# Optimization experiments

Hardware: AMD Instinct MI355X
Metric: run time of the kernel (lower is better)

The kernel has to match this reference:

```python
import jax, jax.numpy as jnp
import numpy as np

MAX_NUM_CAPS = 10
NEG = -1e9

def _layernorm(x, g, b):
    m = x.mean(-1, keepdims=True)
    v = x.var(-1, keepdims=True)
    return (x - m) / jnp.sqrt(v + 1e-5) * g + b

def _gatv2(x, Wl, Wr, att, bias, adj):
    # x: [B,M,F]; Wl/Wr: [F,H*C]; att: [H,C]; adj: [B,M,M] bool, adj[b,i,j] = edge i->j
    B, M, F = x.shape
    H, C = att.shape
    xl = jnp.einsum('bmf,fhc->bmhc', x, Wl.reshape(F, H, C))  # source transform
    xr = jnp.einsum('bmf,fhc->bmhc', x, Wr.reshape(F, H, C))  # target transform
    # GATv2 score: att . leaky_relu(xl[i] + xr[j]) for edge (src=i, dst=j)
    z = jax.nn.leaky_relu(xl[:, :, None, :, :] + xr[:, None, :, :, :], 0.2)  # [B,i,j,H,C]
    e = jnp.einsum('bijhc,hc->bijh', z, att)
    e = jnp.where(adj[..., None], e, NEG)
    alpha = jax.nn.softmax(e, axis=1)  # softmax over incoming sources i per target j
    out = jnp.einsum('bijh,bihc->bjhc', alpha, xl)  # aggregate at targets
    return out.reshape(B, M, H * C) + bias

def setup_inputs() -> dict:
    key = jax.random.key(0)
    ks = jax.random.split(key, 16)
    B, N, T = 128, 16, 48
    Fm, H, C3 = 128, 4, 64
    s = 0.05
    inp = {
        'team_obs': jax.random.normal(ks[0], (B, N, 14), jnp.float32),
        'target_obs': jax.random.normal(ks[1], (B, T, 15), jnp.float32),
        'team_mask': jax.random.normal(ks[2], (B, 2, N), jnp.float32),
        'local_target_mask': jnp.ones((B, T + 1), jnp.float32),
        'W_emb': jax.random.normal(ks[3], (16, Fm), jnp.float32) * s,
        'b_emb': jnp.zeros((Fm,), jnp.float32),
        'Wl1': jax.random.normal(ks[4], (Fm, Fm), jnp.float32) * s,
        'Wr1': jax.random.normal(ks[5], (Fm, Fm), jnp.float32) * s,
        'att1': jax.random.normal(ks[6], (H, Fm // H), jnp.float32) * s,
        'b1': jnp.zeros((Fm,), jnp.float32),
        'Wl2': jax.random.normal(ks[7], (Fm, Fm), jnp.float32) * s,
        'Wr2': jax.random.normal(ks[8], (Fm, Fm), jnp.float32) * s,
        'att2': jax.random.normal(ks[9], (H, Fm // H), jnp.float32) * s,
        'b2': jnp.zeros((Fm,), jnp.float32),
        'Wl3': jax.random.normal(ks[10], (Fm, C3), jnp.float32) * s,
        'Wr3': jax.random.normal(ks[11], (Fm, C3), jnp.float32) * s,
        'att3': jax.random.normal(ks[12], (1, C3), jnp.float32) * s,
        'b3': jnp.zeros((C3,), jnp.float32),
        'ln1_g': jnp.ones((Fm,), jnp.float32),
        'ln1_b': jnp.zeros((Fm,), jnp.float32),
        'ln2_g': jnp.ones((Fm,), jnp.float32),
        'ln2_b': jnp.zeros((Fm,), jnp.float32),
    }
    return inp

def reference(team_obs, target_obs, team_mask, local_target_mask,
              W_emb, b_emb, Wl1, Wr1, att1, b1, Wl2, Wr2, att2, b2,
              Wl3, Wr3, att3, b3, ln1_g, ln1_b, ln2_g, ln2_b):
    B, N, _ = team_obs.shape
    team = jnp.concatenate([team_obs, jnp.zeros((B, N, 2), team_obs.dtype)], axis=2)
    tgt = target_obs[:, :, :-1]
    T = tgt.shape[1]
    tgt = jnp.concatenate([tgt[:, :, :2 + MAX_NUM_CAPS],
                           jnp.zeros((B, T, 2), tgt.dtype),
                           tgt[:, :, -2:]], axis=2)
    fin = jnp.concatenate([team, tgt], axis=1)  # [B, M, inp_dim]
    h = fin @ W_emb + b_emb  # [B, M, 128]
    imp_team = team_mask[:, 0] != -1e9          # [B, N]
    imp_tgt = local_target_mask[:, :-1] != 0.0  # [B, T]
    imp = jnp.concatenate([imp_team, imp_tgt], axis=1)  # [B, M]
    M = N + T
    eye = jnp.eye(M, dtype=bool)
    # edges among active nodes minus diagonal; PyG GATv2Conv add_self_loops=True re-adds self edges
    adj = (imp[:, :, None] & imp[:, None, :] & ~eye) | eye  # [B, M, M]
    out = jax.nn.relu(_layernorm(_gatv2(h, Wl1, Wr1, att1, b1, adj), ln1_g, ln1_b))
    out = jax.nn.relu(_layernorm(_gatv2(out, Wl2, Wr2, att2, b2, adj), ln2_g, ln2_b))
    out = _gatv2(out, Wl3, Wr3, att3, b3, adj)
    return out  # [B, M, out_dim]
```

## Files before the change

kernel.cpp:

```cpp
#include <hip/hip_runtime.h>

typedef unsigned short u16;
typedef unsigned int   u32;
typedef _Float16 h2  __attribute__((ext_vector_type(2)));
typedef __fp16   hw2 __attribute__((ext_vector_type(2)));
typedef __fp16   hw8 __attribute__((ext_vector_type(8)));
typedef float    f4  __attribute__((ext_vector_type(4)));

#define XS 136

static __device__ __forceinline__ h2 pk(float a, float b) {
    return __builtin_bit_cast(h2, __builtin_amdgcn_cvt_pkrtz(a, b));
}
static __device__ __forceinline__ float dot2(h2 a, h2 b, float c) {
    return __builtin_amdgcn_fdot2(__builtin_bit_cast(hw2, a),
                                  __builtin_bit_cast(hw2, b), c, false);
}
static __device__ __forceinline__ h2  b2h(u32 v) { return __builtin_bit_cast(h2, v); }
static __device__ __forceinline__ u32 h2u(h2 v)  { return __builtin_bit_cast(u32, v); }
static __device__ __forceinline__ h2  abs2(h2 v) { return b2h(h2u(v) & 0x7fff7fffu); }
static __device__ __forceinline__ u16 f2h(float f) { return __builtin_bit_cast(u16, (_Float16)f); }
static __device__ __forceinline__ float h2f(u16 v) { return (float)__builtin_bit_cast(_Float16, v); }
static __device__ __forceinline__ f4 mfma16(uint4 a, uint4 b, f4 c) {
    return __builtin_amdgcn_mfma_f32_16x16x32_f16(__builtin_bit_cast(hw8, a),
                                                  __builtin_bit_cast(hw8, b), c, 0, 0, 0);
}
static __device__ __forceinline__ h2 shflx32(h2 v) {
    return b2h((u32)__shfl_xor((int)h2u(v), 32));
}

__global__ void pack_weights(const float* __restrict__ Wl1, const float* __restrict__ Wr1,
                             const float* __restrict__ Wl2, const float* __restrict__ Wr2,
                             const float* __restrict__ Wl3, const float* __restrict__ Wr3,
                             u32* __restrict__ wpk)
{
    const int o = blockIdx.x * 256 + threadIdx.x;
    const float* src; u32* dst; int local; int N;
    if      (o < 8192)  { src = Wl1; dst = wpk;         local = o;         N = 128; }
    else if (o < 16384) { src = Wr1; dst = wpk + 8192;  local = o - 8192;  N = 128; }
    else if (o < 24576) { src = Wl2; dst = wpk + 16384; local = o - 16384; N = 128; }
    else if (o < 32768) { src = Wr2; dst = wpk + 24576; local = o - 24576; N = 128; }
    else if (o < 36864) { src = Wl3; dst = wpk + 32768; local = o - 32768; N = 64;  }
    else                { src = Wr3; dst = wpk + 36864; local = o - 36864; N = 64;  }
    const int i2   = local & 3;
    const int lane = (local >> 2) & 63;
    const int frag = local >> 8;
    const int kb   = frag & 3;
    const int nt   = frag >> 2;
    const int k0   = kb*32 + ((lane >> 4) << 3) + i2*2;
    const int n    = nt*16 + (lane & 15);
    dst[local] = h2u(pk(src[k0*N + n], src[(k0+1)*N + n]));
}

static __device__ __forceinline__ void compute_imp(int t, int b,
    const float* __restrict__ team_mask, const float* __restrict__ ltm, float* sImp)
{
    if (t < 64) {
        float im;
        if (t < 16) im = (team_mask[b*32 + t] != -1000000000.0f) ? 1.f : 0.f;
        else        im = (ltm[b*49 + (t-16)] != 0.0f) ? 1.f : 0.f;
        sImp[t] = im;
    }
}

static __device__ __forceinline__ void matmul128(int w, int lane,
    const u32* __restrict__ wpkL, const u32* __restrict__ wpkR,
    const u16* sX, u16* sXl, uint4* sXrP)
{
    const int  mt  = w & 3;
    const bool isR = (w >= 4);
    const u32* wp  = isR ? wpkR : wpkL;
    const int  n15 = lane & 15;
    const int  qd  = lane >> 4;
    uint4 afr[4];
#pragma unroll
    for (int kb = 0; kb < 4; kb++)
        afr[kb] = *(const uint4*)&sX[(mt*16 + n15)*XS + kb*32 + (qd << 3)];
#pragma unroll
    for (int nt = 0; nt < 8; nt++) {
        f4 acc = {0.f, 0.f, 0.f, 0.f};
#pragma unroll
        for (int kb = 0; kb < 4; kb++) {
            uint4 bf = *(const uint4*)&wp[((nt*4 + kb)*64 + lane)*4];
            acc = mfma16(afr[kb], bf, acc);
        }
        const int n  = nt*16 + n15;
        const int mb = mt*16 + (qd << 2);
        if (!isR) {
#pragma unroll
            for (int r = 0; r < 4; r++) sXl[(mb + r)*XS + n] = f2h(acc[r]);
        } else {
            u16* xp = (u16*)sXrP;
#pragma unroll
            for (int r = 0; r < 4; r++)
                xp[(((n >> 3)*64) + mb + r)*8 + (n & 7)] = f2h(acc[r]);
        }
    }
}

static __device__ __forceinline__ void attn_ln(int t, int w, int lane, int b, int jh,
    const float* __restrict__ att, const float* __restrict__ bias,
    const float* __restrict__ lg, const float* __restrict__ lb,
    u16* sX, const u16* sXl, const uint4* sXrP,
    float* sAl, float* sPart, float* sL2, const float* sImp, u32* __restrict__ gxOut)
{
    const int h  = w & 3;
    const int ih = w >> 2;
    const int jj = lane & 31;
    const int is = lane >> 5;
    const int j  = jh*32 + jj;

    h2 a2[16];
#pragma unroll
    for (int q = 0; q < 16; q++) a2[q] = pk(att[h*32 + 2*q], att[h*32 + 2*q + 1]);

    if (w < 4) {
        const uint4* pr = (const uint4*)&sXl[lane*XS + h*32];
        float al = 0.f;
#pragma unroll
        for (int c4 = 0; c4 < 4; c4++) {
            uint4 v = pr[c4];
            al = dot2(b2h(v.x), a2[c4*4+0], al);
            al = dot2(b2h(v.y), a2[c4*4+1], al);
            al = dot2(b2h(v.z), a2[c4*4+2], al);
            al = dot2(b2h(v.w), a2[c4*4+3], al);
        }
        sAl[h*64 + lane] = al;
    }

    h2 xr2[16];
#pragma unroll
    for (int s = 0; s < 4; s++) {
        uint4 v = sXrP[(h*4 + s)*64 + j];
        xr2[s*4+0] = b2h(v.x); xr2[s*4+1] = b2h(v.y);
        xr2[s*4+2] = b2h(v.z); xr2[s*4+3] = b2h(v.w);
    }
    float Ar = 0.f;
#pragma unroll
    for (int q = 0; q < 16; q++) Ar = dot2(a2[q], xr2[q], Ar);
    const float impj = sImp[j];
    __syncthreads();

    float l = 0.f;
    h2 acc2[16];
#pragma unroll
    for (int q = 0; q < 16; q++) acc2[q] = b2h(0u);
    const int i0 = ih*32 + is*16;
#pragma unroll 4
    for (int ii = 0; ii < 16; ii++) {
        int i = i0 + ii;
        const uint4* pl = (const uint4*)&sXl[i*XS + h*32];
        uint4 v0 = pl[0], v1 = pl[1], v2 = pl[2], v3 = pl[3];
        h2 xl2[16];
        xl2[0] = b2h(v0.x); xl2[1] = b2h(v0.y); xl2[2]  = b2h(v0.z); xl2[3]  = b2h(v0.w);
        xl2[4] = b2h(v1.x); xl2[5] = b2h(v1.y); xl2[6]  = b2h(v1.z); xl2[7]  = b2h(v1.w);
        xl2[8] = b2h(v2.x); xl2[9] = b2h(v2.y); xl2[10] = b2h(v2.z); xl2[11] = b2h(v2.w);
        xl2[12]= b2h(v3.x); xl2[13]= b2h(v3.y); xl2[14] = b2h(v3.z); xl2[15] = b2h(v3.w);
        float S0 = 0.f, S1 = 0.f;
#pragma unroll
        for (int q = 0; q < 16; q += 2) {
            h2 t0 = abs2(xl2[q]   + xr2[q]);
            h2 t1 = abs2(xl2[q+1] + xr2[q+1]);
            S0 = dot2(a2[q],   t0, S0);
            S1 = dot2(a2[q+1], t1, S1);
        }
        float e  = 0.6f*(sAl[h*64 + i] + Ar) + 0.4f*(S0 + S1);
        float ad = (i == j) ? 1.f : impj * sImp[i];
        float p  = (ad != 0.f) ? __expf(e) : 0.f;
        l += p;
        h2 p2 = pk(p, p);
#pragma unroll
        for (int q = 0; q < 16; q++) acc2[q] += p2 * xl2[q];
    }

    l += __shfl_xor(l, 32);
#pragma unroll
    for (int q = 0; q < 16; q++) acc2[q] = acc2[q] + shflx32(acc2[q]);

    u32* ov = (u32*)sX;
    if (w >= 4 && lane < 32) {
        uint4* d4 = (uint4*)(ov + (h*32 + jj)*20);
        uint4 o;
        o.x = h2u(acc2[0]);  o.y = h2u(acc2[1]);  o.z = h2u(acc2[2]);  o.w = h2u(acc2[3]);  d4[0] = o;
        o.x = h2u(acc2[4]);  o.y = h2u(acc2[5]);  o.z = h2u(acc2[6]);  o.w = h2u(acc2[7]);  d4[1] = o;
        o.x = h2u(acc2[8]);  o.y = h2u(acc2[9]);  o.z = h2u(acc2[10]); o.w = h2u(acc2[11]); d4[2] = o;
        o.x = h2u(acc2[12]); o.y = h2u(acc2[13]); o.z = h2u(acc2[14]); o.w = h2u(acc2[15]); d4[3] = o;
        sL2[h*32 + jj] = l;
    }
    __syncthreads();

    float yv[32];
    if (w < 4 && lane < 32) {
        const uint4* s4 = (const uint4*)(ov + (h*32 + jj)*20);
        uint4 u0 = s4[0], u1 = s4[1], u2 = s4[2], u3 = s4[3];
        h2 oth[16];
        oth[0] = b2h(u0.x); oth[1] = b2h(u0.y); oth[2]  = b2h(u0.z); oth[3]  = b2h(u0.w);
        oth[4] = b2h(u1.x); oth[5] = b2h(u1.y); oth[6]  = b2h(u1.z); oth[7]  = b2h(u1.w);
        oth[8] = b2h(u2.x); oth[9] = b2h(u2.y); oth[10] = b2h(u2.z); oth[11] = b2h(u2.w);
        oth[12]= b2h(u3.x); oth[13]= b2h(u3.y); oth[14] = b2h(u3.z); oth[15] = b2h(u3.w);
        l += sL2[h*32 + jj];
        const float rl = 1.f / l;
        float s1 = 0.f, s2v = 0.f;
#pragma unroll
        for (int q = 0; q < 16; q++) {
            h2 sum = acc2[q] + oth[q];
            float y0 = fmaf((float)sum[0], rl, bias[h*32 + 2*q]);
            float y1 = fmaf((float)sum[1], rl, bias[h*32 + 2*q + 1]);
            yv[2*q] = y0; yv[2*q+1] = y1;
            s1 += y0 + y1;
            s2v = fmaf(y0, y0, s2v);
            s2v = fmaf(y1, y1, s2v);
        }
        sPart[h*32 + jj]       = s1;
        sPart[128 + h*32 + jj] = s2v;
    }
    __syncthreads();

    if (w < 4 && lane < 32) {
        float su = sPart[jj] + sPart[32 + jj] + sPart[64 + jj] + sPart[96 + jj];
        float sq = sPart[128 + jj] + sPart[160 + jj] + sPart[192 + jj] + sPart[224 + jj];
        const float mean = su * 0.0078125f;
        const float var  = sq * 0.0078125f - mean*mean;
        const float rstd = rsqrtf(var + 1e-5f);
#pragma unroll
        for (int q = 0; q < 16; q++) {
            int f0 = h*32 + 2*q;
            float v0 = fmaxf(fmaf((yv[2*q]   - mean)*rstd, lg[f0],   lb[f0]),   0.f);
            float v1 = fmaxf(fmaf((yv[2*q+1] - mean)*rstd, lg[f0+1], lb[f0+1]), 0.f);
            ov[(h*32 + jj)*20 + q] = h2u(pk(v0, v1));
        }
    }
    __syncthreads();

    for (int r = t; r < 2048; r += 512) {
        int nj = r >> 6, c = r & 63, hh = c >> 4, qq = c & 15;
        gxOut[(size_t)b*4096 + (size_t)(jh*32 + nj)*64 + c] = ov[(hh*32 + nj)*20 + qq];
    }
}

__global__ void __launch_bounds__(512, 1) gnn_layer1(
    const float* __restrict__ team_obs, const float* __restrict__ target_obs,
    const float* __restrict__ team_mask, const float* __restrict__ ltm,
    const float* __restrict__ W_emb, const float* __restrict__ b_emb,
    const float* __restrict__ att1, const float* __restrict__ b1,
    const float* __restrict__ ln1_g, const float* __restrict__ ln1_b,
    const u32* __restrict__ wpk, u32* __restrict__ gx1)
{
    __shared__ __align__(16) u16   sX  [64*XS];
    __shared__ __align__(16) u16   sXl [64*XS];
    __shared__ __align__(16) uint4 sXrP[1024];
    __shared__ float sFin[1024];
    __shared__ float sAl [256];
    __shared__ float sPart[256];
    __shared__ float sL2 [128];
    __shared__ float sImp[64];

    const int t    = threadIdx.x;
    const int w    = t >> 6;
    const int lane = t & 63;
    const int b    = blockIdx.x >> 1;
    const int jh   = blockIdx.x & 1;

    compute_imp(t, b, team_mask, ltm, sImp);
    for (int ee = t; ee < 1024; ee += 512) {
        int m = ee >> 4, k = ee & 15;
        float v = 0.f;
        if (m < 16) {
            if (k < 14) v = team_obs[(b*16 + m)*14 + k];
        } else {
            const float* tg = target_obs + (size_t)(b*48 + (m-16))*15;
            if      (k < 12)  v = tg[k];
            else if (k == 14) v = tg[12];
            else if (k == 15) v = tg[13];
        }
        sFin[m*16 + k] = v;
    }
    __syncthreads();

    {
        const int f = t & 127;
        const int g = t >> 7;
        float wreg[16];
#pragma unroll
        for (int k = 0; k < 16; k++) wreg[k] = W_emb[k*128 + f];
        const float bf = b_emb[f];
#pragma unroll
        for (int mm = 0; mm < 16; mm++) {
            int m = g*16 + mm;
            const float4* pf = (const float4*)&sFin[m*16];
            float4 f0 = pf[0], f1 = pf[1], f2 = pf[2], f3 = pf[3];
            float acc = bf;
            acc = fmaf(f0.x, wreg[0],  acc); acc = fmaf(f0.y, wreg[1],  acc);
            acc = fmaf(f0.z, wreg[2],  acc); acc = fmaf(f0.w, wreg[3],  acc);
            acc = fmaf(f1.x, wreg[4],  acc); acc = fmaf(f1.y, wreg[5],  acc);
            acc = fmaf(f1.z, wreg[6],  acc); acc = fmaf(f1.w, wreg[7],  acc);
            acc = fmaf(f2.x, wreg[8],  acc); acc = fmaf(f2.y, wreg[9],  acc);
            acc = fmaf(f2.z, wreg[10], acc); acc = fmaf(f2.w, wreg[11], acc);
            acc = fmaf(f3.x, wreg[12], acc); acc = fmaf(f3.y, wreg[13], acc);
            acc = fmaf(f3.z, wreg[14], acc); acc = fmaf(f3.w, wreg[15], acc);
            sX[m*XS + f] = f2h(acc);
        }
    }
    __syncthreads();

    matmul128(w, lane, wpk, wpk + 8192, sX, sXl, sXrP);
    __syncthreads();
    attn_ln(t, w, lane, b, jh, att1, b1, ln1_g, ln1_b,
            sX, sXl, sXrP, sAl, sPart, sL2, sImp, gx1);
}

__global__ void __launch_bounds__(512, 1) gnn_layer2(
    const float* __restrict__ team_mask, const float* __restrict__ ltm,
    const float* __restrict__ att2, const float* __restrict__ b2,
    const float* __restrict__ ln2_g, const float* __restrict__ ln2_b,
    const u32* __restrict__ wpk, const u32* __restrict__ gxIn, u32* __restrict__ gxOut)
{
    __shared__ __align__(16) u16   sX  [64*XS];
    __shared__ __align__(16) u16   sXl [64*XS];
    __shared__ __align__(16) uint4 sXrP[1024];
    __shared__ float sAl [256];
    __shared__ float sPart[256];
    __shared__ float sL2 [128];
    __shared__ float sImp[64];

    const int t    = threadIdx.x;
    const int w    = t >> 6;
    const int lane = t & 63;
    const int b    = blockIdx.x >> 1;
    const int jh   = blockIdx.x & 1;

    compute_imp(t, b, team_mask, ltm, sImp);
    const uint4* gin = (const uint4*)(gxIn + (size_t)b*4096);
    for (int r = t; r < 1024; r += 512) {
        uint4 v = gin[r];
        int m = r >> 4, seg = r & 15;
        *(uint4*)&sX[m*XS + seg*8] = v;
    }
    __syncthreads();

    matmul128(w, lane, wpk + 16384, wpk + 24576, sX, sXl, sXrP);
    __syncthreads();
    attn_ln(t, w, lane, b, jh, att2, b2, ln2_g, ln2_b,
            sX, sXl, sXrP, sAl, sPart, sL2, sImp, gxOut);
}

__global__ void __launch_bounds__(512, 1) gnn_layer3(
    const float* __restrict__ team_mask, const float* __restrict__ ltm,
    const float* __restrict__ att3, const float* __restrict__ b3,
    const u32* __restrict__ wpk, const u32* __restrict__ gxIn, float* __restrict__ out)
{
    __shared__ __align__(16) u16   sX  [64*XS];
    __shared__ __align__(16) u16   sXl [64*XS];
    __shared__ __align__(16) uint4 sXrP[512];
    __shared__ float sAl [64];
    __shared__ float sPart[512];
    __shared__ float sImp[64];
    __shared__ u16   sE  [64*32];

    const int t    = threadIdx.x;
    const int w    = t >> 6;
    const int lane = t & 63;
    const int b    = blockIdx.x >> 1;
    const int jh   = blockIdx.x & 1;

    compute_imp(t, b, team_mask, ltm, sImp);
    const uint4* gin = (const uint4*)(gxIn + (size_t)b*4096);
    for (int r = t; r < 1024; r += 512) {
        uint4 v = gin[r];
        int m = r >> 4, seg = r & 15;
        *(uint4*)&sX[m*XS + seg*8] = v;
    }
    __syncthreads();

    {
        const int  mt  = w & 3;
        const bool isR = (w >= 4);
        const u32* wp  = isR ? (wpk + 36864) : (wpk + 32768);
        const int  n15 = lane & 15;
        const int  qd  = lane >> 4;
        uint4 afr[4];
#pragma unroll
        for (int kb = 0; kb < 4; kb++)
            afr[kb] = *(const uint4*)&sX[(mt*16 + n15)*XS + kb*32 + (qd << 3)];
#pragma unroll
        for (int nt = 0; nt < 4; nt++) {
            f4 acc = {0.f, 0.f, 0.f, 0.f};
#pragma unroll
            for (int kb = 0; kb < 4; kb++) {
                uint4 bf = *(const uint4*)&wp[((nt*4 + kb)*64 + lane)*4];
                acc = mfma16(afr[kb], bf, acc);
            }
            const int n  = nt*16 + n15;
            const int mb = mt*16 + (qd << 2);
            if (!isR) {
#pragma unroll
                for (int r = 0; r < 4; r++) sXl[(mb + r)*XS + n] = f2h(acc[r]);
            } else {
                u16* xp = (u16*)sXrP;
#pragma unroll
                for (int r = 0; r < 4; r++)
                    xp[(((n >> 3)*64) + mb + r)*8 + (n & 7)] = f2h(acc[r]);
            }
        }
    }
    __syncthreads();

    {
        h2 a2l[4];
#pragma unroll
        for (int q = 0; q < 4; q++) a2l[q] = pk(att3[w*8 + 2*q], att3[w*8 + 2*q + 1]);
        uint4 v = *(const uint4*)&sXl[lane*XS + w*8];
        float al = 0.f;
        al = dot2(b2h(v.x), a2l[0], al);
        al = dot2(b2h(v.y), a2l[1], al);
        al = dot2(b2h(v.z), a2l[2], al);
        al = dot2(b2h(v.w), a2l[3], al);
        sPart[w*64 + lane] = al;
    }
    __syncthreads();
    if (t < 64) {
        sAl[t] = ((sPart[t] + sPart[64+t]) + (sPart[128+t] + sPart[192+t]))
               + ((sPart[256+t] + sPart[320+t]) + (sPart[384+t] + sPart[448+t]));
    }
    __syncthreads();

    const int jj = lane & 31;
    const int is = lane >> 5;
    const int j  = jh*32 + jj;

    {
        h2 a3[32], xr3[32];
#pragma unroll
        for (int q = 0; q < 32; q++) a3[q] = pk(att3[2*q], att3[2*q + 1]);
#pragma unroll
        for (int s = 0; s < 8; s++) {
            uint4 v = sXrP[s*64 + j];
            xr3[s*4+0] = b2h(v.x); xr3[s*4+1] = b2h(v.y);
            xr3[s*4+2] = b2h(v.z); xr3[s*4+3] = b2h(v.w);
        }
        float Ar = 0.f;
#pragma unroll
        for (int q = 0; q < 32; q++) Ar = dot2(a3[q], xr3[q], Ar);
        const float impj = sImp[j];
        const int ib = (w*2 + is)*4;
        for (int ii = 0; ii < 4; ii++) {
            int i = ib + ii;
            const uint4* pl = (const uint4*)&sXl[i*XS];
            float S0 = 0.f, S1 = 0.f;
#pragma unroll
            for (int c4 = 0; c4 < 8; c4++) {
                uint4 v = pl[c4];
                S0 = dot2(a3[c4*4+0], abs2(b2h(v.x) + xr3[c4*4+0]), S0);
                S1 = dot2(a3[c4*4+1], abs2(b2h(v.y) + xr3[c4*4+1]), S1);
                S0 = dot2(a3[c4*4+2], abs2(b2h(v.z) + xr3[c4*4+2]), S0);
                S1 = dot2(a3[c4*4+3], abs2(b2h(v.w) + xr3[c4*4+3]), S1);
            }
            float e  = 0.6f*(sAl[i] + Ar) + 0.4f*(S0 + S1);
            float ad = (i == j) ? 1.f : impj * sImp[i];
            e = (ad != 0.f) ? e : -60000.0f;
            sE[i*32 + jj] = f2h(e);
        }
    }
    __syncthreads();

    {
        const int c0 = w*8;
        h2 acc2[4];
#pragma unroll
        for (int q = 0; q < 4; q++) acc2[q] = b2h(0u);
        float l = 0.f;
        for (int k = 0; k < 32; k++) {
            int i = is*32 + k;
            float p = __expf(h2f(sE[i*32 + jj]));
            l += p;
            h2 p2 = pk(p, p);
            uint4 v = *(const uint4*)&sXl[i*XS + c0];
            acc2[0] += p2 * b2h(v.x);
            acc2[1] += p2 * b2h(v.y);
            acc2[2] += p2 * b2h(v.z);
            acc2[3] += p2 * b2h(v.w);
        }
        l += __shfl_xor(l, 32);
#pragma unroll
        for (int q = 0; q < 4; q++) acc2[q] = acc2[q] + shflx32(acc2[q]);
        if (is == 0) {
            const float rl = 1.f / l;
            float o[8];
#pragma unroll
            for (int q = 0; q < 4; q++) {
                o[2*q]   = fmaf((float)acc2[q][0], rl, b3[c0 + 2*q]);
                o[2*q+1] = fmaf((float)acc2[q][1], rl, b3[c0 + 2*q + 1]);
            }
            float4* po = (float4*)(out + (size_t)b*4096 + (size_t)j*64 + c0);
            po[0] = *(const float4*)&o[0];
            po[1] = *(const float4*)&o[4];
        }
    }
}

extern "C" void kernel_launch(void* const* d_in, const int* in_sizes, int n_in,
                              void* d_out, int out_size, void* d_ws, size_t ws_size,
                              hipStream_t stream) {
    (void)in_sizes; (void)n_in; (void)ws_size; (void)out_size;
    const float* team_obs          = (const float*)d_in[0];
    const float* target_obs        = (const float*)d_in[1];
    const float* team_mask         = (const float*)d_in[2];
    const float* local_target_mask = (const float*)d_in[3];
    const float* W_emb             = (const float*)d_in[4];
    const float* b_emb             = (const float*)d_in[5];
    const float* Wl1               = (const float*)d_in[6];
    const float* Wr1               = (const float*)d_in[7];
    const float* att1              = (const float*)d_in[8];
    const float* b1                = (const float*)d_in[9];
    const float* Wl2               = (const float*)d_in[10];
    const float* Wr2               = (const float*)d_in[11];
    const float* att2              = (const float*)d_in[12];
    const float* b2                = (const float*)d_in[13];
    const float* Wl3               = (const float*)d_in[14];
    const float* Wr3               = (const float*)d_in[15];
    const float* att3              = (const float*)d_in[16];
    const float* b3                = (const float*)d_in[17];
    const float* ln1_g             = (const float*)d_in[18];
    const float* ln1_b             = (const float*)d_in[19];
    const float* ln2_g             = (const float*)d_in[20];
    const float* ln2_b             = (const float*)d_in[21];
    float* out = (float*)d_out;

    u32* wpk = (u32*)d_ws;
    u32* gx2 = (u32*)d_ws + 40960;
    u32* gx1 = (u32*)d_out;

    pack_weights<<<dim3(160), dim3(256), 0, stream>>>(Wl1, Wr1, Wl2, Wr2, Wl3, Wr3, wpk);
    gnn_layer1<<<dim3(256), dim3(512), 0, stream>>>(
        team_obs, target_obs, team_mask, local_target_mask, W_emb, b_emb,
        att1, b1, ln1_g, ln1_b, wpk, gx1);
    gnn_layer2<<<dim3(256), dim3(512), 0, stream>>>(
        team_mask, local_target_mask, att2, b2, ln2_g, ln2_b, wpk, gx1, gx2);
    gnn_layer3<<<dim3(256), dim3(512), 0, stream>>>(
        team_mask, local_target_mask, att3, b3, wpk, gx2, out);
}
```

Before: 138.6 us.

## Split each batch graph across four blocks instead of two for more parallelism

Each block now handles 16 target nodes instead of 32, so the grid doubles to 512 blocks per layer. Source nodes are split across four lane groups, with a two-step xor-shuffle reduction. Launch bounds are raised to 4 blocks per CU to allow higher occupancy. The price is duplicated per-block work: each block still computes the full 64-node Xl/Xr matmul and the self-attention terms, so redundant compute doubles. The tighter register budget may also cause spills.

New measurement: 192.3 us. +38.7%, slower.

```diff
diff --git a/kernel.cpp b/kernel.cpp
--- a/kernel.cpp
+++ b/kernel.cpp
@@ -25,8 +25,8 @@
     return __builtin_amdgcn_mfma_f32_16x16x32_f16(__builtin_bit_cast(hw8, a),
                                                   __builtin_bit_cast(hw8, b), c, 0, 0, 0);
 }
-static __device__ __forceinline__ h2 shflx32(h2 v) {
-    return b2h((u32)__shfl_xor((int)h2u(v), 32));
+static __device__ __forceinline__ h2 shflx(h2 v, int m) {
+    return b2h((u32)__shfl_xor((int)h2u(v), m));
 }
 
 __global__ void pack_weights(const float* __restrict__ Wl1, const float* __restrict__ Wr1,
@@ -98,7 +98,7 @@
     }
 }
 
-static __device__ __forceinline__ void attn_ln(int t, int w, int lane, int b, int jh,
+static __device__ __forceinline__ void attn_ln(int t, int w, int lane, int b, int jq,
     const float* __restrict__ att, const float* __restrict__ bias,
     const float* __restrict__ lg, const float* __restrict__ lb,
     u16* sX, const u16* sXl, const uint4* sXrP,
@@ -106,9 +106,9 @@
 {
     const int h  = w & 3;
     const int ih = w >> 2;
-    const int jj = lane & 31;
-    const int is = lane >> 5;
-    const int j  = jh*32 + jj;
+    const int jj = lane & 15;
+    const int is = lane >> 4;
+    const int j  = jq*16 + jj;
 
     h2 a2[16];
 #pragma unroll
@@ -145,10 +145,10 @@
     h2 acc2[16];
 #pragma unroll
     for (int q = 0; q < 16; q++) acc2[q] = b2h(0u);
-    const int i0 = ih*32 + is*16;
-#pragma unroll 4
-    for (int ii = 0; ii < 16; ii++) {
-        int i = i0 + ii;
+    const int i0 = ih*32 + is;
+#pragma unroll
+    for (int ii = 0; ii < 8; ii++) {
+        int i = i0 + ii*4;
         const uint4* pl = (const uint4*)&sXl[i*XS + h*32];
         uint4 v0 = pl[0], v1 = pl[1], v2 = pl[2], v3 = pl[3];
         h2 xl2[16];
@@ -173,32 +173,32 @@
         for (int q = 0; q < 16; q++) acc2[q] += p2 * xl2[q];
     }
 
-    l += __shfl_xor(l, 32);
-#pragma unroll
-    for (int q = 0; q < 16; q++) acc2[q] = acc2[q] + shflx32(acc2[q]);
+    l += __shfl_xor(l, 16); l += __shfl_xor(l, 32);
+#pragma unroll
+    for (int q = 0; q < 16; q++) { acc2[q] += shflx(acc2[q], 16); acc2[q] += shflx(acc2[q], 32); }
 
     u32* ov = (u32*)sX;
-    if (w >= 4 && lane < 32) {
-        uint4* d4 = (uint4*)(ov + (h*32 + jj)*20);
+    if (w >= 4 && lane < 16) {
+        uint4* d4 = (uint4*)(ov + (h*16 + jj)*20);
         uint4 o;
         o.x = h2u(acc2[0]);  o.y = h2u(acc2[1]);  o.z = h2u(acc2[2]);  o.w = h2u(acc2[3]);  d4[0] = o;
         o.x = h2u(acc2[4]);  o.y = h2u(acc2[5]);  o.z = h2u(acc2[6]);  o.w = h2u(acc2[7]);  d4[1] = o;
         o.x = h2u(acc2[8]);  o.y = h2u(acc2[9]);  o.z = h2u(acc2[10]); o.w = h2u(acc2[11]); d4[2] = o;
         o.x = h2u(acc2[12]); o.y = h2u(acc2[13]); o.z = h2u(acc2[14]); o.w = h2u(acc2[15]); d4[3] = o;
-        sL2[h*32 + jj] = l;
+        sL2[h*16 + jj] = l;
     }
     __syncthreads();
 
     float yv[32];
-    if (w < 4 && lane < 32) {
-        const uint4* s4 = (const uint4*)(ov + (h*32 + jj)*20);
+    if (w < 4 && lane < 16) {
+        const uint4* s4 = (const uint4*)(ov + (h*16 + jj)*20);
         uint4 u0 = s4[0], u1 = s4[1], u2 = s4[2], u3 = s4[3];
         h2 oth[16];
         oth[0] = b2h(u0.x); oth[1] = b2h(u0.y); oth[2]  = b2h(u0.z); oth[3]  = b2h(u0.w);
         oth[4] = b2h(u1.x); oth[5] = b2h(u1.y); oth[6]  = b2h(u1.z); oth[7]  = b2h(u1.w);
         oth[8] = b2h(u2.x); oth[9] = b2h(u2.y); oth[10] = b2h(u2.z); oth[11] = b2h(u2.w);
         oth[12]= b2h(u3.x); oth[13]= b2h(u3.y); oth[14] = b2h(u3.z); oth[15] = b2h(u3.w);
-        l += sL2[h*32 + jj];
+        l += sL2[h*16 + jj];
         const float rl = 1.f / l;
         float s1 = 0.f, s2v = 0.f;
 #pragma unroll
@@ -211,14 +211,14 @@
             s2v = fmaf(y0, y0, s2v);
             s2v = fmaf(y1, y1, s2v);
         }
-        sPart[h*32 + jj]       = s1;
-        sPart[128 + h*32 + jj] = s2v;
-    }
-    __syncthreads();
-
-    if (w < 4 && lane < 32) {
-        float su = sPart[jj] + sPart[32 + jj] + sPart[64 + jj] + sPart[96 + jj];
-        float sq = sPart[128 + jj] + sPart[160 + jj] + sPart[192 + jj] + sPart[224 + jj];
+        sPart[h*16 + jj]      = s1;
+        sPart[64 + h*16 + jj] = s2v;
+    }
+    __syncthreads();
+
+    if (w < 4 && lane < 16) {
+        float su = sPart[jj] + sPart[16 + jj] + sPart[32 + jj] + sPart[48 + jj];
+        float sq = sPart[64 + jj] + sPart[80 + jj] + sPart[96 + jj] + sPart[112 + jj];
         const float mean = su * 0.0078125f;
         const float var  = sq * 0.0078125f - mean*mean;
         const float rstd = rsqrtf(var + 1e-5f);
@@ -227,18 +227,18 @@
             int f0 = h*32 + 2*q;
             float v0 = fmaxf(fmaf((yv[2*q]   - mean)*rstd, lg[f0],   lb[f0]),   0.f);
             float v1 = fmaxf(fmaf((yv[2*q+1] - mean)*rstd, lg[f0+1], lb[f0+1]), 0.f);
-            ov[(h*32 + jj)*20 + q] = h2u(pk(v0, v1));
-        }
-    }
-    __syncthreads();
-
-    for (int r = t; r < 2048; r += 512) {
+            ov[(h*16 + jj)*20 + q] = h2u(pk(v0, v1));
+        }
+    }
+    __syncthreads();
+
+    for (int r = t; r < 1024; r += 512) {
         int nj = r >> 6, c = r & 63, hh = c >> 4, qq = c & 15;
-        gxOut[(size_t)b*4096 + (size_t)(jh*32 + nj)*64 + c] = ov[(hh*32 + nj)*20 + qq];
-    }
-}
-
-__global__ void __launch_bounds__(512, 1) gnn_layer1(
+        gxOut[(size_t)b*4096 + (size_t)(jq*16 + nj)*64 + c] = ov[(hh*16 + nj)*20 + qq];
+    }
+}
+
+__global__ void __launch_bounds__(512, 4) gnn_layer1(
     const float* __restrict__ team_obs, const float* __restrict__ target_obs,
     const float* __restrict__ team_mask, const float* __restrict__ ltm,
     const float* __restrict__ W_emb, const float* __restrict__ b_emb,
@@ -251,15 +251,15 @@
     __shared__ __align__(16) uint4 sXrP[1024];
     __shared__ float sFin[1024];
     __shared__ float sAl [256];
-    __shared__ float sPart[256];
-    __shared__ float sL2 [128];
+    __shared__ float sPart[128];
+    __shared__ float sL2 [64];
     __shared__ float sImp[64];
 
     const int t    = threadIdx.x;
     const int w    = t >> 6;
     const int lane = t & 63;
-    const int b    = blockIdx.x >> 1;
-    const int jh   = blockIdx.x & 1;
+    const int b    = blockIdx.x >> 2;
+    const int jq   = blockIdx.x & 3;
 
     compute_imp(t, b, team_mask, ltm, sImp);
     for (int ee = t; ee < 1024; ee += 512) {
@@ -305,11 +305,11 @@
 
     matmul128(w, lane, wpk, wpk + 8192, sX, sXl, sXrP);
     __syncthreads();
-    attn_ln(t, w, lane, b, jh, att1, b1, ln1_g, ln1_b,
+    attn_ln(t, w, lane, b, jq, att1, b1, ln1_g, ln1_b,
             sX, sXl, sXrP, sAl, sPart, sL2, sImp, gx1);
 }
 
-__global__ void __launch_bounds__(512, 1) gnn_layer2(
+__global__ void __launch_bounds__(512, 4) gnn_layer2(
     const float* __restrict__ team_mask, const float* __restrict__ ltm,
     const float* __restrict__ att2, const float* __restrict__ b2,
     const float* __restrict__ ln2_g, const float* __restrict__ ln2_b,
@@ -319,15 +319,15 @@
     __shared__ __align__(16) u16   sXl [64*XS];
     __shared__ __align__(16) uint4 sXrP[1024];
     __shared__ float sAl [256];
-    __shared__ float sPart[256];
-    __shared__ float sL2 [128];
+    __shared__ float sPart[128];
+    __shared__ float sL2 [64];
     __shared__ float sImp[64];
 
     const int t    = threadIdx.x;
     const int w    = t >> 6;
     const int lane = t & 63;
-    const int b    = blockIdx.x >> 1;
-    const int jh   = blockIdx.x & 1;
+    const int b    = blockIdx.x >> 2;
+    const int jq   = blockIdx.x & 3;
 
     compute_imp(t, b, team_mask, ltm, sImp);
     const uint4* gin = (const uint4*)(gxIn + (size_t)b*4096);
@@ -340,11 +340,11 @@
 
     matmul128(w, lane, wpk + 16384, wpk + 24576, sX, sXl, sXrP);
     __syncthreads();
-    attn_ln(t, w, lane, b, jh, att2, b2, ln2_g, ln2_b,
+    attn_ln(t, w, lane, b, jq, att2, b2, ln2_g, ln2_b,
             sX, sXl, sXrP, sAl, sPart, sL2, sImp, gxOut);
 }
 
-__global__ void __launch_bounds__(512, 1) gnn_layer3(
+__global__ void __launch_bounds__(512, 4) gnn_layer3(
     const float* __restrict__ team_mask, const float* __restrict__ ltm,
     const float* __restrict__ att3, const float* __restrict__ b3,
     const u32* __restrict__ wpk, const u32* __restrict__ gxIn, float* __restrict__ out)
@@ -355,13 +355,13 @@
     __shared__ float sAl [64];
     __shared__ float sPart[512];
     __shared__ float sImp[64];
-    __shared__ u16   sE  [64*32];
+    __shared__ u16   sE  [64*16];
 
     const int t    = threadIdx.x;
     const int w    = t >> 6;
     const int lane = t & 63;
-    const int b    = blockIdx.x >> 1;
-    const int jh   = blockIdx.x & 1;
+    const int b    = blockIdx.x >> 2;
+    const int jq   = blockIdx.x & 3;
 
     compute_imp(t, b, team_mask, ltm, sImp);
     const uint4* gin = (const uint4*)(gxIn + (size_t)b*4096);
@@ -424,9 +424,9 @@
     }
     __syncthreads();
 
-    const int jj = lane & 31;
-    const int is = lane >> 5;
-    const int j  = jh*32 + jj;
+    const int jj = lane & 15;
+    const int is = lane >> 4;
+    const int j  = jq*16 + jj;
 
     {
         h2 a3[32], xr3[32];
@@ -442,8 +442,9 @@
 #pragma unroll
         for (int q = 0; q < 32; q++) Ar = dot2(a3[q], xr3[q], Ar);
         const float impj = sImp[j];
-        const int ib = (w*2 + is)*4;
-        for (int ii = 0; ii < 4; ii++) {
+        const int ib = (w*4 + is)*2;
+#pragma unroll
+        for (int ii = 0; ii < 2; ii++) {
             int i = ib + ii;
             const uint4* pl = (const uint4*)&sXl[i*XS];
             float S0 = 0.f, S1 = 0.f;
@@ -458,7 +459,7 @@
             float e  = 0.6f*(sAl[i] + Ar) + 0.4f*(S0 + S1);
             float ad = (i == j) ? 1.f : impj * sImp[i];
             e = (ad != 0.f) ? e : -60000.0f;
-            sE[i*32 + jj] = f2h(e);
+            sE[i*16 + jj] = f2h(e);
         }
     }
     __syncthreads();
@@ -469,9 +470,9 @@
 #pragma unroll
         for (int q = 0; q < 4; q++) acc2[q] = b2h(0u);
         float l = 0.f;
-        for (int k = 0; k < 32; k++) {
-            int i = is*32 + k;
-            float p = __expf(h2f(sE[i*32 + jj]));
+        for (int k = 0; k < 16; k++) {
+            int i = is + 4*k;
+            float p = __expf(h2f(sE[i*16 + jj]));
             l += p;
             h2 p2 = pk(p, p);
             uint4 v = *(const uint4*)&sXl[i*XS + c0];
@@ -480,9 +481,9 @@
             acc2[2] += p2 * b2h(v.z);
             acc2[3] += p2 * b2h(v.w);
         }
-        l += __shfl_xor(l, 32);
-#pragma unroll
-        for (int q = 0; q < 4; q++) acc2[q] = acc2[q] + shflx32(acc2[q]);
+        l += __shfl_xor(l, 16); l += __shfl_xor(l, 32);
+#pragma unroll
+        for (int q = 0; q < 4; q++) { acc2[q] += shflx(acc2[q], 16); acc2[q] += shflx(acc2[q], 32); }
         if (is == 0) {
             const float rl = 1.f / l;
             float o[8];
@@ -531,11 +532,11 @@
     u32* gx1 = (u32*)d_out;
 
     pack_weights<<<dim3(160), dim3(256), 0, stream>>>(Wl1, Wr1, Wl2, Wr2, Wl3, Wr3, wpk);
-    gnn_layer1<<<dim3(256), dim3(512), 0, stream>>>(
+    gnn_layer1<<<dim3(512), dim3(512), 0, stream>>>(
         team_obs, target_obs, team_mask, local_target_mask, W_emb, b_emb,
         att1, b1, ln1_g, ln1_b, wpk, gx1);
-    gnn_layer2<<<dim3(256), dim3(512), 0, stream>>>(
+    gnn_layer2<<<dim3(512), dim3(512), 0, stream>>>(
         team_mask, local_target_mask, att2, b2, ln2_g, ln2_b, wpk, gx1, gx2);
-    gnn_layer3<<<dim3(256), dim3(512), 0, stream>>>(
+    gnn_layer3<<<dim3(512), dim3(512), 0, stream>>>(
         team_mask, local_target_mask, att3, b3, wpk, gx2, out);
 }
```

## Fuse three GNN layer kernels into one cooperative kernel with grid syncs

Applied to the files above, without the earlier changes.

Merges the three per-layer kernels into a single cooperative launch, using grid-wide barriers between layers instead of separate kernel launches. This removes two kernel launch gaps and the per-kernel mask recomputation. The layer-3 score buffer reuses the sFin shared array, and the intermediates move from the output buffer to workspace. In exchange the kernel pays grid.sync costs and must have all 256 blocks co-resident, and shared-memory usage now becomes the union of all three layers.

Measured after the change: 220.6 us. +59.1%, slower.

```diff
diff --git a/kernel.cpp b/kernel.cpp
--- a/kernel.cpp
+++ b/kernel.cpp
@@ -1,4 +1,7 @@
 #include <hip/hip_runtime.h>
+#include <hip/hip_cooperative_groups.h>
+
+namespace cg = cooperative_groups;
 
 typedef unsigned short u16;
 typedef unsigned int   u32;
@@ -52,17 +55,6 @@
     dst[local] = h2u(pk(src[k0*N + n], src[(k0+1)*N + n]));
 }
 
-static __device__ __forceinline__ void compute_imp(int t, int b,
-    const float* __restrict__ team_mask, const float* __restrict__ ltm, float* sImp)
-{
-    if (t < 64) {
-        float im;
-        if (t < 16) im = (team_mask[b*32 + t] != -1000000000.0f) ? 1.f : 0.f;
-        else        im = (ltm[b*49 + (t-16)] != 0.0f) ? 1.f : 0.f;
-        sImp[t] = im;
-    }
-}
-
 static __device__ __forceinline__ void matmul128(int w, int lane,
     const u32* __restrict__ wpkL, const u32* __restrict__ wpkR,
     const u16* sX, u16* sXl, uint4* sXrP)
@@ -238,22 +230,28 @@
     }
 }
 
-__global__ void __launch_bounds__(512, 1) gnn_layer1(
+__global__ void __launch_bounds__(512) gnn_all(
     const float* __restrict__ team_obs, const float* __restrict__ target_obs,
     const float* __restrict__ team_mask, const float* __restrict__ ltm,
     const float* __restrict__ W_emb, const float* __restrict__ b_emb,
     const float* __restrict__ att1, const float* __restrict__ b1,
+    const float* __restrict__ att2, const float* __restrict__ b2,
+    const float* __restrict__ att3, const float* __restrict__ b3,
     const float* __restrict__ ln1_g, const float* __restrict__ ln1_b,
-    const u32* __restrict__ wpk, u32* __restrict__ gx1)
+    const float* __restrict__ ln2_g, const float* __restrict__ ln2_b,
+    const u32* __restrict__ wpk, u32* __restrict__ gx1, u32* __restrict__ gx2,
+    float* __restrict__ out)
 {
     __shared__ __align__(16) u16   sX  [64*XS];
     __shared__ __align__(16) u16   sXl [64*XS];
     __shared__ __align__(16) uint4 sXrP[1024];
-    __shared__ float sFin[1024];
+    __shared__ __align__(16) float sFin[1024];
     __shared__ float sAl [256];
-    __shared__ float sPart[256];
+    __shared__ float sPart[512];
     __shared__ float sL2 [128];
     __shared__ float sImp[64];
+
+    cg::grid_group grid = cg::this_grid();
 
     const int t    = threadIdx.x;
     const int w    = t >> 6;
@@ -261,7 +259,12 @@
     const int b    = blockIdx.x >> 1;
     const int jh   = blockIdx.x & 1;
 
-    compute_imp(t, b, team_mask, ltm, sImp);
+    if (t < 64) {
+        float im;
+        if (t < 16) im = (team_mask[b*32 + t] != -1000000000.0f) ? 1.f : 0.f;
+        else        im = (ltm[b*49 + (t-16)] != 0.0f) ? 1.f : 0.f;
+        sImp[t] = im;
+    }
     for (int ee = t; ee < 1024; ee += 512) {
         int m = ee >> 4, k = ee & 15;
         float v = 0.f;
@@ -307,68 +310,30 @@
     __syncthreads();
     attn_ln(t, w, lane, b, jh, att1, b1, ln1_g, ln1_b,
             sX, sXl, sXrP, sAl, sPart, sL2, sImp, gx1);
-}
-
-__global__ void __launch_bounds__(512, 1) gnn_layer2(
-    const float* __restrict__ team_mask, const float* __restrict__ ltm,
-    const float* __restrict__ att2, const float* __restrict__ b2,
-    const float* __restrict__ ln2_g, const float* __restrict__ ln2_b,
-    const u32* __restrict__ wpk, const u32* __restrict__ gxIn, u32* __restrict__ gxOut)
-{
-    __shared__ __align__(16) u16   sX  [64*XS];
-    __shared__ __align__(16) u16   sXl [64*XS];
-    __shared__ __align__(16) uint4 sXrP[1024];
-    __shared__ float sAl [256];
-    __shared__ float sPart[256];
-    __shared__ float sL2 [128];
-    __shared__ float sImp[64];
-
-    const int t    = threadIdx.x;
-    const int w    = t >> 6;
-    const int lane = t & 63;
-    const int b    = blockIdx.x >> 1;
-    const int jh   = blockIdx.x & 1;
-
-    compute_imp(t, b, team_mask, ltm, sImp);
-    const uint4* gin = (const uint4*)(gxIn + (size_t)b*4096);
-    for (int r = t; r < 1024; r += 512) {
-        uint4 v = gin[r];
-        int m = r >> 4, seg = r & 15;
-        *(uint4*)&sX[m*XS + seg*8] = v;
-    }
-    __syncthreads();
-
+    grid.sync();
+
+    {
+        const uint4* gin = (const uint4*)(gx1 + (size_t)b*4096);
+        for (int r = t; r < 1024; r += 512) {
+            uint4 v = gin[r];
+            int m = r >> 4, seg = r & 15;
+            *(uint4*)&sX[m*XS + seg*8] = v;
+        }
+    }
+    __syncthreads();
     matmul128(w, lane, wpk + 16384, wpk + 24576, sX, sXl, sXrP);
     __syncthreads();
     attn_ln(t, w, lane, b, jh, att2, b2, ln2_g, ln2_b,
-            sX, sXl, sXrP, sAl, sPart, sL2, sImp, gxOut);
-}
-
-__global__ void __launch_bounds__(512, 1) gnn_layer3(
-    const float* __restrict__ team_mask, const float* __restrict__ ltm,
-    const float* __restrict__ att3, const float* __restrict__ b3,
-    const u32* __restrict__ wpk, const u32* __restrict__ gxIn, float* __restrict__ out)
-{
-    __shared__ __align__(16) u16   sX  [64*XS];
-    __shared__ __align__(16) u16   sXl [64*XS];
-    __shared__ __align__(16) uint4 sXrP[512];
-    __shared__ float sAl [64];
-    __shared__ float sPart[512];
-    __shared__ float sImp[64];
-    __shared__ u16   sE  [64*32];
-
-    const int t    = threadIdx.x;
-    const int w    = t >> 6;
-    const int lane = t & 63;
-    const int b    = blockIdx.x >> 1;
-    const int jh   = blockIdx.x & 1;
-
-    compute_imp(t, b, team_mask, ltm, sImp);
-    const uint4* gin = (const uint4*)(gxIn + (size_t)b*4096);
-    for (int r = t; r < 1024; r += 512) {
-        uint4 v = gin[r];
-        int m = r >> 4, seg = r & 15;
-        *(uint4*)&sX[m*XS + seg*8] = v;
+            sX, sXl, sXrP, sAl, sPart, sL2, sImp, gx2);
+    grid.sync();
+
+    {
+        const uint4* gin = (const uint4*)(gx2 + (size_t)b*4096);
+        for (int r = t; r < 1024; r += 512) {
+            uint4 v = gin[r];
+            int m = r >> 4, seg = r & 15;
+            *(uint4*)&sX[m*XS + seg*8] = v;
+        }
     }
     __syncthreads();
 
@@ -424,76 +389,79 @@
     }
     __syncthreads();
 
-    const int jj = lane & 31;
-    const int is = lane >> 5;
-    const int j  = jh*32 + jj;
-
     {
-        h2 a3[32], xr3[32];
-#pragma unroll
-        for (int q = 0; q < 32; q++) a3[q] = pk(att3[2*q], att3[2*q + 1]);
-#pragma unroll
-        for (int s = 0; s < 8; s++) {
-            uint4 v = sXrP[s*64 + j];
-            xr3[s*4+0] = b2h(v.x); xr3[s*4+1] = b2h(v.y);
-            xr3[s*4+2] = b2h(v.z); xr3[s*4+3] = b2h(v.w);
-        }
-        float Ar = 0.f;
-#pragma unroll
-        for (int q = 0; q < 32; q++) Ar = dot2(a3[q], xr3[q], Ar);
-        const float impj = sImp[j];
-        const int ib = (w*2 + is)*4;
-        for (int ii = 0; ii < 4; ii++) {
-            int i = ib + ii;
-            const uint4* pl = (const uint4*)&sXl[i*XS];
-            float S0 = 0.f, S1 = 0.f;
-#pragma unroll
-            for (int c4 = 0; c4 < 8; c4++) {
-                uint4 v = pl[c4];
-                S0 = dot2(a3[c4*4+0], abs2(b2h(v.x) + xr3[c4*4+0]), S0);
-                S1 = dot2(a3[c4*4+1], abs2(b2h(v.y) + xr3[c4*4+1]), S1);
-                S0 = dot2(a3[c4*4+2], abs2(b2h(v.z) + xr3[c4*4+2]), S0);
-                S1 = dot2(a3[c4*4+3], abs2(b2h(v.w) + xr3[c4*4+3]), S1);
+        const int jj = lane & 31;
+        const int is = lane >> 5;
+        const int j  = jh*32 + jj;
+        u16* sE = (u16*)sFin;
+
+        {
+            h2 a3[32], xr3[32];
+#pragma unroll
+            for (int q = 0; q < 32; q++) a3[q] = pk(att3[2*q], att3[2*q + 1]);
+#pragma unroll
+            for (int s = 0; s < 8; s++) {
+                uint4 v = sXrP[s*64 + j];
+                xr3[s*4+0] = b2h(v.x); xr3[s*4+1] = b2h(v.y);
+                xr3[s*4+2] = b2h(v.z); xr3[s*4+3] = b2h(v.w);
             }
-            float e  = 0.6f*(sAl[i] + Ar) + 0.4f*(S0 + S1);
-            float ad = (i == j) ? 1.f : impj * sImp[i];
-            e = (ad != 0.f) ? e : -60000.0f;
-            sE[i*32 + jj] = f2h(e);
-        }
-    }
-    __syncthreads();
-
-    {
-        const int c0 = w*8;
-        h2 acc2[4];
-#pragma unroll
-        for (int q = 0; q < 4; q++) acc2[q] = b2h(0u);
-        float l = 0.f;
-        for (int k = 0; k < 32; k++) {
-            int i = is*32 + k;
-            float p = __expf(h2f(sE[i*32 + jj]));
-            l += p;
-            h2 p2 = pk(p, p);
-            uint4 v = *(const uint4*)&sXl[i*XS + c0];
-            acc2[0] += p2 * b2h(v.x);
-            acc2[1] += p2 * b2h(v.y);
-            acc2[2] += p2 * b2h(v.z);
-            acc2[3] += p2 * b2h(v.w);
-        }
-        l += __shfl_xor(l, 32);
-#pragma unroll
-        for (int q = 0; q < 4; q++) acc2[q] = acc2[q] + shflx32(acc2[q]);
-        if (is == 0) {
-            const float rl = 1.f / l;
-            float o[8];
-#pragma unroll
-            for (int q = 0; q < 4; q++) {
-                o[2*q]   = fmaf((float)acc2[q][0], rl, b3[c0 + 2*q]);
-                o[2*q+1] = fmaf((float)acc2[q][1], rl, b3[c0 + 2*q + 1]);
+            float Ar = 0.f;
+#pragma unroll
+            for (int q = 0; q < 32; q++) Ar = dot2(a3[q], xr3[q], Ar);
+            const float impj = sImp[j];
+            const int ib = (w*2 + is)*4;
+            for (int ii = 0; ii < 4; ii++) {
+                int i = ib + ii;
+                const uint4* pl = (const uint4*)&sXl[i*XS];
+                float S0 = 0.f, S1 = 0.f;
+#pragma unroll
+                for (int c4 = 0; c4 < 8; c4++) {
+                    uint4 v = pl[c4];
+                    S0 = dot2(a3[c4*4+0], abs2(b2h(v.x) + xr3[c4*4+0]), S0);
+                    S1 = dot2(a3[c4*4+1], abs2(b2h(v.y) + xr3[c4*4+1]), S1);
+                    S0 = dot2(a3[c4*4+2], abs2(b2h(v.z) + xr3[c4*4+2]), S0);
+                    S1 = dot2(a3[c4*4+3], abs2(b2h(v.w) + xr3[c4*4+3]), S1);
+                }
+                float e  = 0.6f*(sAl[i] + Ar) + 0.4f*(S0 + S1);
+                float ad = (i == j) ? 1.f : impj * sImp[i];
+                e = (ad != 0.f) ? e : -60000.0f;
+                sE[i*32 + jj] = f2h(e);
             }
-            float4* po = (float4*)(out + (size_t)b*4096 + (size_t)j*64 + c0);
-            po[0] = *(const float4*)&o[0];
-            po[1] = *(const float4*)&o[4];
+        }
+        __syncthreads();
+
+        {
+            const int c0 = w*8;
+            h2 acc2[4];
+#pragma unroll
+            for (int q = 0; q < 4; q++) acc2[q] = b2h(0u);
+            float l = 0.f;
+            for (int k = 0; k < 32; k++) {
+                int i = is*32 + k;
+                float p = __expf(h2f(sE[i*32 + jj]));
+                l += p;
+                h2 p2 = pk(p, p);
+                uint4 v = *(const uint4*)&sXl[i*XS + c0];
+                acc2[0] += p2 * b2h(v.x);
+                acc2[1] += p2 * b2h(v.y);
+                acc2[2] += p2 * b2h(v.z);
+                acc2[3] += p2 * b2h(v.w);
+            }
+            l += __shfl_xor(l, 32);
+#pragma unroll
+            for (int q = 0; q < 4; q++) acc2[q] = acc2[q] + shflx32(acc2[q]);
+            if (is == 0) {
+                const float rl = 1.f / l;
+                float o[8];
+#pragma unroll
+                for (int q = 0; q < 4; q++) {
+                    o[2*q]   = fmaf((float)acc2[q][0], rl, b3[c0 + 2*q]);
+                    o[2*q+1] = fmaf((float)acc2[q][1], rl, b3[c0 + 2*q + 1]);
+                }
+                float4* po = (float4*)(out + (size_t)b*4096 + (size_t)j*64 + c0);
+                po[0] = *(const float4*)&o[0];
+                po[1] = *(const float4*)&o[4];
+            }
         }
     }
 }
@@ -527,15 +495,17 @@
     float* out = (float*)d_out;
 
     u32* wpk = (u32*)d_ws;
-    u32* gx2 = (u32*)d_ws + 40960;
-    u32* gx1 = (u32*)d_out;
+    u32* gx1 = (u32*)d_ws + 40960;
+    u32* gx2 = (u32*)d_ws + 40960 + 524288;
 
     pack_weights<<<dim3(160), dim3(256), 0, stream>>>(Wl1, Wr1, Wl2, Wr2, Wl3, Wr3, wpk);
-    gnn_layer1<<<dim3(256), dim3(512), 0, stream>>>(
-        team_obs, target_obs, team_mask, local_target_mask, W_emb, b_emb,
-        att1, b1, ln1_g, ln1_b, wpk, gx1);
-    gnn_layer2<<<dim3(256), dim3(512), 0, stream>>>(
-        team_mask, local_target_mask, att2, b2, ln2_g, ln2_b, wpk, gx1, gx2);
-    gnn_layer3<<<dim3(256), dim3(512), 0, stream>>>(
-        team_mask, local_target_mask, att3, b3, wpk, gx2, out);
-}
+
+    void* args[] = {
+        (void*)&team_obs, (void*)&target_obs, (void*)&team_mask, (void*)&local_target_mask,
+        (void*)&W_emb, (void*)&b_emb,
+        (void*)&att1, (void*)&b1, (void*)&att2, (void*)&b2, (void*)&att3, (void*)&b3,
+        (void*)&ln1_g, (void*)&ln1_b, (void*)&ln2_g, (void*)&ln2_b,
+        (void*)&wpk, (void*)&gx1, (void*)&gx2, (void*)&out
+    };
+    hipLaunchCooperativeKernel((void*)gnn_all, dim3(256), dim3(512), args, 0, stream);
+}
```

## Load matmul A-fragments from global directly and write layer outputs straight to global

Applied to the files above, without the earlier changes.

Layers 2 and 3 now read MFMA A-fragments directly from the global activation buffer instead of first staging them into shared memory, which removes a copy loop and a barrier. The layernorm epilogue writes each row to global with vector stores from registers, replacing the shared-memory transpose, a barrier and a strided copy loop. The block-index mapping also changes so that the two half-blocks of a batch sit 128 blocks apart rather than adjacent. The cost is less coalesced global reads for fragments, and in layer 2 the attention stage still receives the sX buffer, which is no longer filled.

Result: no change. 139.0 us, median of 2 (+0.2%).

```diff
diff --git a/kernel.cpp b/kernel.cpp
--- a/kernel.cpp
+++ b/kernel.cpp
@@ -98,6 +98,42 @@
     }
 }
 
+static __device__ __forceinline__ void matmul128g(int w, int lane,
+    const u32* __restrict__ wpkL, const u32* __restrict__ wpkR,
+    const u32* __restrict__ gxRow, u16* sXl, uint4* sXrP)
+{
+    const int  mt  = w & 3;
+    const bool isR = (w >= 4);
+    const u32* wp  = isR ? wpkR : wpkL;
+    const int  n15 = lane & 15;
+    const int  qd  = lane >> 4;
+    const int  m   = mt*16 + n15;
+    uint4 afr[4];
+#pragma unroll
+    for (int kb = 0; kb < 4; kb++)
+        afr[kb] = *(const uint4*)&gxRow[m*64 + kb*16 + qd*4];
+#pragma unroll
+    for (int nt = 0; nt < 8; nt++) {
+        f4 acc = {0.f, 0.f, 0.f, 0.f};
+#pragma unroll
+        for (int kb = 0; kb < 4; kb++) {
+            uint4 bf = *(const uint4*)&wp[((nt*4 + kb)*64 + lane)*4];
+            acc = mfma16(afr[kb], bf, acc);
+        }
+        const int n  = nt*16 + n15;
+        const int mb = mt*16 + (qd << 2);
+        if (!isR) {
+#pragma unroll
+            for (int r = 0; r < 4; r++) sXl[(mb + r)*XS + n] = f2h(acc[r]);
+        } else {
+            u16* xp = (u16*)sXrP;
+#pragma unroll
+            for (int r = 0; r < 4; r++)
+                xp[(((n >> 3)*64) + mb + r)*8 + (n & 7)] = f2h(acc[r]);
+        }
+    }
+}
+
 static __device__ __forceinline__ void attn_ln(int t, int w, int lane, int b, int jh,
     const float* __restrict__ att, const float* __restrict__ bias,
     const float* __restrict__ lg, const float* __restrict__ lb,
@@ -222,19 +258,19 @@
         const float mean = su * 0.0078125f;
         const float var  = sq * 0.0078125f - mean*mean;
         const float rstd = rsqrtf(var + 1e-5f);
+        u32 orow[16];
 #pragma unroll
         for (int q = 0; q < 16; q++) {
             int f0 = h*32 + 2*q;
             float v0 = fmaxf(fmaf((yv[2*q]   - mean)*rstd, lg[f0],   lb[f0]),   0.f);
             float v1 = fmaxf(fmaf((yv[2*q+1] - mean)*rstd, lg[f0+1], lb[f0+1]), 0.f);
-            ov[(h*32 + jj)*20 + q] = h2u(pk(v0, v1));
-        }
-    }
-    __syncthreads();
-
-    for (int r = t; r < 2048; r += 512) {
-        int nj = r >> 6, c = r & 63, hh = c >> 4, qq = c & 15;
-        gxOut[(size_t)b*4096 + (size_t)(jh*32 + nj)*64 + c] = ov[(hh*32 + nj)*20 + qq];
+            orow[q] = h2u(pk(v0, v1));
+        }
+        uint4* po = (uint4*)(gxOut + (size_t)b*4096 + (size_t)j*64 + h*16);
+        po[0] = *(uint4*)&orow[0];
+        po[1] = *(uint4*)&orow[4];
+        po[2] = *(uint4*)&orow[8];
+        po[3] = *(uint4*)&orow[12];
     }
 }
 
@@ -258,8 +294,8 @@
     const int t    = threadIdx.x;
     const int w    = t >> 6;
     const int lane = t & 63;
-    const int b    = blockIdx.x >> 1;
-    const int jh   = blockIdx.x & 1;
+    const int b    = blockIdx.x & 127;
+    const int jh   = blockIdx.x >> 7;
 
     compute_imp(t, b, team_mask, ltm, sImp);
     for (int ee = t; ee < 1024; ee += 512) {
@@ -326,19 +362,11 @@
     const int t    = threadIdx.x;
     const int w    = t >> 6;
     const int lane = t & 63;
-    const int b    = blockIdx.x >> 1;
-    const int jh   = blockIdx.x & 1;
+    const int b    = blockIdx.x & 127;
+    const int jh   = blockIdx.x >> 7;
 
     compute_imp(t, b, team_mask, ltm, sImp);
-    const uint4* gin = (const uint4*)(gxIn + (size_t)b*4096);
-    for (int r = t; r < 1024; r += 512) {
-        uint4 v = gin[r];
-        int m = r >> 4, seg = r & 15;
-        *(uint4*)&sX[m*XS + seg*8] = v;
-    }
-    __syncthreads();
-
-    matmul128(w, lane, wpk + 16384, wpk + 24576, sX, sXl, sXrP);
+    matmul128g(w, lane, wpk + 16384, wpk + 24576, gxIn + (size_t)b*4096, sXl, sXrP);
     __syncthreads();
     attn_ln(t, w, lane, b, jh, att2, b2, ln2_g, ln2_b,
             sX, sXl, sXrP, sAl, sPart, sL2, sImp, gxOut);
@@ -349,7 +377,6 @@
     const float* __restrict__ att3, const float* __restrict__ b3,
     const u32* __restrict__ wpk, const u32* __restrict__ gxIn, float* __restrict__ out)
 {
-    __shared__ __align__(16) u16   sX  [64*XS];
     __shared__ __align__(16) u16   sXl [64*XS];
     __shared__ __align__(16) uint4 sXrP[512];
     __shared__ float sAl [64];
@@ -360,17 +387,11 @@
     const int t    = threadIdx.x;
     const int w    = t >> 6;
     const int lane = t & 63;
-    const int b    = blockIdx.x >> 1;
-    const int jh   = blockIdx.x & 1;
+    const int b    = blockIdx.x & 127;
+    const int jh   = blockIdx.x >> 7;
 
     compute_imp(t, b, team_mask, ltm, sImp);
-    const uint4* gin = (const uint4*)(gxIn + (size_t)b*4096);
-    for (int r = t; r < 1024; r += 512) {
-        uint4 v = gin[r];
-        int m = r >> 4, seg = r & 15;
-        *(uint4*)&sX[m*XS + seg*8] = v;
-    }
-    __syncthreads();
+    const u32* gxRow = gxIn + (size_t)b*4096;
 
     {
         const int  mt  = w & 3;
@@ -378,10 +399,11 @@
         const u32* wp  = isR ? (wpk + 36864) : (wpk + 32768);
         const int  n15 = lane & 15;
         const int  qd  = lane >> 4;
+        const int  m   = mt*16 + n15;
         uint4 afr[4];
 #pragma unroll
         for (int kb = 0; kb < 4; kb++)
-            afr[kb] = *(const uint4*)&sX[(mt*16 + n15)*XS + kb*32 + (qd << 3)];
+            afr[kb] = *(const uint4*)&gxRow[m*64 + kb*16 + qd*4];
 #pragma unroll
         for (int nt = 0; nt < 4; nt++) {
             f4 acc = {0.f, 0.f, 0.f, 0.f};
```
